# Performance work log

Measured on AMD Instinct MI355X. Metric: run time of the kernel, lower is better.

## Reference

```python
import jax, jax.numpy as jnp
import numpy as np

HIDDEN = 2048
FFN = 1024
NUM_EXPERTS = 64
TOP_K = 8
TOTAL_EXPERTS = NUM_EXPERTS + TOP_K  # trash-can experts appended


def setup_inputs() -> dict:
    key = jax.random.key(0)
    ks = jax.random.split(key, 5)
    hidden_states = jax.random.normal(ks[0], (4, 2048, HIDDEN), dtype=jnp.float32)
    # gate: [total_experts, hidden]
    gate_w = jax.random.normal(ks[1], (TOTAL_EXPERTS, HIDDEN), dtype=jnp.float32) * 0.02
    # OlmoeMLP (SwiGLU): gate_proj, up_proj: [E, hidden, ffn]; down_proj: [E, ffn, hidden]
    w_gate = jax.random.normal(ks[2], (NUM_EXPERTS, HIDDEN, FFN), dtype=jnp.float32) * 0.02
    w_up = jax.random.normal(ks[3], (NUM_EXPERTS, HIDDEN, FFN), dtype=jnp.float32) * 0.02
    w_down = jax.random.normal(ks[4], (NUM_EXPERTS, FFN, HIDDEN), dtype=jnp.float32) * 0.02
    return {"hidden_states": hidden_states, "gate_w": gate_w,
            "w_gate": w_gate, "w_up": w_up, "w_down": w_down}


def _moe_forward(hidden_states, gate_w, w_gate, w_up, w_down):
    b, s, h = hidden_states.shape
    x = hidden_states.reshape(-1, h)  # [T, H]
    router_logits = x @ gate_w.T  # [T, total_experts]
    routing_weights = jax.nn.softmax(router_logits.astype(jnp.float32), axis=-1)
    topk_w, topk_idx = jax.lax.top_k(routing_weights, TOP_K)  # [T, K]
    # norm_topk_prob = False -> no renorm
    topk_w = topk_w.astype(hidden_states.dtype)

    # Dense-equivalent combine honoring sparsity via per-expert mask-weighted sum:
    # combine_w[t, e] = sum of topk weights where topk_idx==e, zero for trash experts.
    onehot = jax.nn.one_hot(topk_idx, TOTAL_EXPERTS, dtype=topk_w.dtype)  # [T,K,E_tot]
    combine_w = jnp.einsum('tk,tke->te', topk_w, onehot)[:, :NUM_EXPERTS]  # [T,E]

    # Grouped expert compute (vectorized over experts).
    # For correctness baseline we compute each expert on all tokens and weight;
    # zero weights kill non-routed tokens (same math as gather/scatter).
    def one_expert(wg, wu, wd, w_col):
        inter = jax.nn.silu(x @ wg) * (x @ wu)  # [T, FFN]
        return (inter @ wd) * w_col[:, None]    # [T, H]

    out = jnp.zeros_like(x)
    # scan over experts to cap peak memory at one [T,FFN] intermediate
    def body(acc, args):
        wg, wu, wd, w_col = args
        return acc + one_expert(wg, wu, wd, w_col), None
    out, _ = jax.lax.scan(body, out, (w_gate, w_up, w_down, combine_w.T))
    return out.reshape(b, s, h), router_logits


def reference(hidden_states, gate_w, w_gate, w_up, w_down):
    return _moe_forward(hidden_states, gate_w, w_gate, w_up, w_down)
```

## Files before the change

### kernel.cpp

```cpp
#include <hip/hip_runtime.h>
#include <hip/hip_bf16.h>
#include <stdint.h>

#define T_TOK 8192
#define HID   2048
#define FFN   1024
#define NEXP  64
#define ETOT  72
#define NPAD  80
#define TOPK  8
#define NASSIGN (T_TOK*TOPK)

typedef unsigned short u16;
typedef __bf16 bf16;
typedef bf16 bf16x8 __attribute__((ext_vector_type(8)));
typedef float f32x4 __attribute__((ext_vector_type(4)));

typedef const __attribute__((address_space(1))) void* gp_t;
typedef __attribute__((address_space(3))) void* lp_t;

__device__ __forceinline__ void gload16(const void* g, void* lds) {
  __builtin_amdgcn_global_load_lds((gp_t)g, (lp_t)lds, 16, 0, 0);
}
__device__ __forceinline__ f32x4 mfma16(bf16x8 a, bf16x8 b, f32x4 c) {
  return __builtin_amdgcn_mfma_f32_16x16x32_bf16(a, b, c, 0, 0, 0);
}

union U8 { bf16 h[8]; uint4 u; };
union U2 { bf16 h[2]; unsigned int u; };

__global__ void k_prep_x(const float* __restrict__ x, u16* __restrict__ xh,
                         u16* __restrict__ xl, int n8) {
  int i = blockIdx.x * blockDim.x + threadIdx.x;
  int stride = gridDim.x * blockDim.x;
  for (; i < n8; i += stride) {
    const float4* p = (const float4*)(x + (size_t)i * 8);
    float4 a = p[0], b = p[1];
    float f[8] = {a.x,a.y,a.z,a.w,b.x,b.y,b.z,b.w};
    U8 hh, ll;
#pragma unroll
    for (int j = 0; j < 8; j++) {
      bf16 h = (bf16)f[j];
      hh.h[j] = h;
      ll.h[j] = (bf16)(f[j] - (float)h);
    }
    ((uint4*)xh)[i] = hh.u;
    ((uint4*)xl)[i] = ll.u;
  }
}

__global__ void k_prep_gate(const float* __restrict__ gw, u16* __restrict__ gh,
                            u16* __restrict__ gl) {
  int e = blockIdx.x;
  for (int k8 = threadIdx.x; k8 < HID/8; k8 += blockDim.x) {
    U8 hh, ll;
    if (e < ETOT) {
      const float4* p = (const float4*)(gw + (size_t)e*HID + k8*8);
      float4 a = p[0], b = p[1];
      float f[8] = {a.x,a.y,a.z,a.w,b.x,b.y,b.z,b.w};
#pragma unroll
      for (int j = 0; j < 8; j++) {
        bf16 h = (bf16)f[j]; hh.h[j] = h; ll.h[j] = (bf16)(f[j]-(float)h);
      }
    } else {
      hh.u = make_uint4(0,0,0,0); ll.u = make_uint4(0,0,0,0);
    }
    ((uint4*)gh)[(size_t)e*(HID/8) + k8] = hh.u;
    ((uint4*)gl)[(size_t)e*(HID/8) + k8] = ll.u;
  }
}

__global__ void k_convT(const float* __restrict__ src, u16* __restrict__ dst,
                        int R, int C) {
  int e = blockIdx.z;
  src += (size_t)e * R * C;
  dst += (size_t)e * R * C;
  int c0 = blockIdx.x * 64, r0 = blockIdx.y * 128;
  __shared__ u16 t[64 * 132];
  int tid = threadIdx.x;
  int rr = tid >> 4, cc = (tid & 15) * 4;
#pragma unroll
  for (int it = 0; it < 8; it++) {
    int r = it * 16 + rr;
    float4 v = *(const float4*)(src + (size_t)(r0 + r) * C + c0 + cc);
    const float* f = &v.x;
#pragma unroll
    for (int i = 0; i < 4; i++) {
      U2 u; u.h[0] = (bf16)f[i]; u.h[1] = (bf16)0.f;
      t[(cc + i) * 132 + r] = (u16)(u.u & 0xffffu);
    }
  }
  __syncthreads();
  int n = tid >> 2, kb = (tid & 3) * 32;
  u16* drow = dst + (size_t)(c0 + n) * R + r0 + kb;
  const u16* srow = &t[n * 132 + kb];
#pragma unroll
  for (int j = 0; j < 2; j++) {
    uint2 a = *(const uint2*)&srow[j*16 + 0];
    uint2 b = *(const uint2*)&srow[j*16 + 4];
    uint2 c = *(const uint2*)&srow[j*16 + 8];
    uint2 d = *(const uint2*)&srow[j*16 + 12];
    *(uint4*)&drow[j*16]     = make_uint4(a.x, a.y, b.x, b.y);
    *(uint4*)&drow[j*16 + 8] = make_uint4(c.x, c.y, d.x, d.y);
  }
}

__global__ void k_router(const u16* __restrict__ xh, const u16* __restrict__ xl,
                         const u16* __restrict__ gh, const u16* __restrict__ gl,
                         float* __restrict__ logits_out, int* __restrict__ tk_idx,
                         float* __restrict__ tk_w, int* __restrict__ counts) {
  __shared__ u16 la_h[64*32], la_l[64*32], lb_h[NPAD*32], lb_l[NPAD*32];
  __shared__ float llog[64*NPAD];
  int tid = threadIdx.x, lane = tid & 63, wid = tid >> 6;
  int t0 = blockIdx.x * 64;
  int rsub = lane >> 2, csub = lane & 3;
  f32x4 acc[5] = {};
#pragma unroll 1
  for (int k0 = 0; k0 < HID; k0 += 32) {
    int arow = wid*16 + rsub;
    gload16(xh + (size_t)(t0+arow)*HID + k0 + csub*8, &la_h[wid*512]);
    gload16(xl + (size_t)(t0+arow)*HID + k0 + csub*8, &la_l[wid*512]);
    int brow = wid*16 + rsub;
    gload16(gh + (size_t)brow*HID + k0 + csub*8, &lb_h[wid*512]);
    gload16(gl + (size_t)brow*HID + k0 + csub*8, &lb_l[wid*512]);
    if (wid == 0) gload16(gh + (size_t)(64+rsub)*HID + k0 + csub*8, &lb_h[4*512]);
    if (wid == 1) gload16(gl + (size_t)(64+rsub)*HID + k0 + csub*8, &lb_l[4*512]);
    __syncthreads();
    int ar = wid*16 + (lane & 15);
    int ks = lane >> 4;
    bf16x8 ah = *(const bf16x8*)&la_h[ar*32 + ks*8];
    bf16x8 al = *(const bf16x8*)&la_l[ar*32 + ks*8];
#pragma unroll
    for (int nf = 0; nf < 5; nf++) {
      int br = nf*16 + (lane & 15);
      bf16x8 bh = *(const bf16x8*)&lb_h[br*32 + ks*8];
      bf16x8 bl = *(const bf16x8*)&lb_l[br*32 + ks*8];
      acc[nf] = mfma16(ah, bh, acc[nf]);
      acc[nf] = mfma16(ah, bl, acc[nf]);
      acc[nf] = mfma16(al, bh, acc[nf]);
    }
    __syncthreads();
  }
  {
    int q = lane >> 4, c = lane & 15;
#pragma unroll
    for (int nf = 0; nf < 5; nf++)
#pragma unroll
      for (int r = 0; r < 4; r++)
        llog[(wid*16 + q*4 + r)*NPAD + nf*16 + c] = acc[nf][r];
  }
  __syncthreads();
  if (tid < 64) {
    int t = t0 + tid;
    float* lg = &llog[tid*NPAD];
    float m = -1e30f;
    for (int e = 0; e < ETOT; e++) {
      float v = lg[e];
      logits_out[(size_t)t*ETOT + e] = v;
      m = fmaxf(m, v);
    }
    float s = 0.f;
    for (int e = 0; e < ETOT; e++) s += __expf(lg[e] - m);
    uint64_t m0 = 0; unsigned int m1 = 0;
    for (int k = 0; k < TOPK; k++) {
      float best = -1e30f; int bi = 0;
      for (int e = 0; e < ETOT; e++) {
        bool used = (e < 64) ? ((m0 >> e) & 1) : ((m1 >> (e-64)) & 1);
        float v = lg[e];
        if (!used && v > best) { best = v; bi = e; }
      }
      if (bi < 64) m0 |= (1ull << bi); else m1 |= (1u << (bi-64));
      tk_idx[t*TOPK + k] = bi;
      tk_w[t*TOPK + k] = __expf(best - m) / s;
      if (bi < NEXP) atomicAdd(&counts[bi], 1);
    }
  }
}

__global__ void k_scan(const int* __restrict__ counts, int* __restrict__ offsets,
                       int* __restrict__ cursors) {
  if (threadIdx.x == 0) {
    int s = 0;
    for (int e = 0; e < NEXP; e++) { offsets[e] = s; cursors[e] = s; s += counts[e]; }
  }
}

__global__ void k_build(const int* __restrict__ tk_idx, const float* __restrict__ tk_w,
                        int* __restrict__ cursors, int* __restrict__ rows,
                        float* __restrict__ rwgt) {
  int t = blockIdx.x * blockDim.x + threadIdx.x;
  if (t >= T_TOK) return;
#pragma unroll
  for (int k = 0; k < TOPK; k++) {
    int e = tk_idx[t*TOPK + k];
    if (e < NEXP) {
      int p = atomicAdd(&cursors[e], 1);
      rows[p] = t;
      rwgt[p] = tk_w[t*TOPK + k];
    }
  }
}

__launch_bounds__(256, 3)
__global__ void k_expert_gu(const u16* __restrict__ xh, const u16* __restrict__ wgT,
                            const u16* __restrict__ wuT, const int* __restrict__ counts,
                            const int* __restrict__ offsets, const int* __restrict__ rows,
                            u16* __restrict__ inter) {
  int wgid = blockIdx.x;
  int xcd = wgid & 7, slot = wgid >> 3;
  int m = slot & 7, q = slot >> 3;
  int g = xcd * 64 + q;
  int e = g >> 3, nb = g & 7;
  int cnt = counts[e];
  if (cnt == 0) return;
  int off = offsets[e];
  int n0 = nb * 128;
  int tid = threadIdx.x, lane = tid & 63, wid = tid >> 6;
  int wm = (wid >> 1) * 64, wn = (wid & 1) * 64;
  __shared__ u16 la[128*32], lbg[128*32], lbu[128*32];
  __shared__ u16 lout[64*128];
  int rsub = lane >> 2, csub = lane & 3;
  int swzc = csub ^ ((rsub >> 1) & 3);
  int nr1 = wid*16 + rsub, nr2 = nr1 + 64;
  const u16* gb_g1 = wgT + ((size_t)e*FFN + n0 + nr1)*HID + swzc*8;
  const u16* gb_g2 = wgT + ((size_t)e*FFN + n0 + nr2)*HID + swzc*8;
  const u16* gb_u1 = wuT + ((size_t)e*FFN + n0 + nr1)*HID + swzc*8;
  const u16* gb_u2 = wuT + ((size_t)e*FFN + n0 + nr2)*HID + swzc*8;

  for (int m0 = m * 128; m0 < cnt; m0 += 1024) {
    int tok1 = (m0 + nr1 < cnt) ? rows[off + m0 + nr1] : 0;
    int tok2 = (m0 + nr2 < cnt) ? rows[off + m0 + nr2] : 0;
    const u16* ga1 = xh + (size_t)tok1*HID + swzc*8;
    const u16* ga2 = xh + (size_t)tok2*HID + swzc*8;
    f32x4 accg[4][4] = {}, accu[4][4] = {};
#pragma unroll 1
    for (int k0 = 0; k0 < HID; k0 += 32) {
      gload16(ga1 + k0, &la[wid*512]);
      gload16(ga2 + k0, &la[(wid+4)*512]);
      gload16(gb_g1 + k0, &lbg[wid*512]);
      gload16(gb_g2 + k0, &lbg[(wid+4)*512]);
      gload16(gb_u1 + k0, &lbu[wid*512]);
      gload16(gb_u2 + k0, &lbu[(wid+4)*512]);
      __syncthreads();
      bf16x8 afr[4], bgf[4], buf_[4];
#pragma unroll
      for (int i = 0; i < 4; i++) {
        int row = wm + i*16 + (lane & 15);
        int ch = (lane >> 4) ^ ((row >> 1) & 3);
        afr[i] = *(const bf16x8*)&la[row*32 + ch*8];
        int n = wn + i*16 + (lane & 15);
        int chb = (lane >> 4) ^ ((n >> 1) & 3);
        bgf[i]  = *(const bf16x8*)&lbg[n*32 + chb*8];
        buf_[i] = *(const bf16x8*)&lbu[n*32 + chb*8];
      }
#pragma unroll
      for (int nf = 0; nf < 4; nf++)
#pragma unroll
        for (int mf = 0; mf < 4; mf++) {
          accg[mf][nf] = mfma16(afr[mf], bgf[nf], accg[mf][nf]);
          accu[mf][nf] = mfma16(afr[mf], buf_[nf], accu[mf][nf]);
        }
      __syncthreads();
    }
#pragma unroll
    for (int pass = 0; pass < 2; pass++) {
      if ((wid >> 1) == pass) {
#pragma unroll
        for (int mf = 0; mf < 4; mf++)
#pragma unroll
          for (int nf = 0; nf < 4; nf++)
#pragma unroll
            for (int r = 0; r < 4; r++) {
              float gg = accg[mf][nf][r], uu = accu[mf][nf][r];
              float v = gg / (1.f + __expf(-gg)) * uu;
              int row = mf*16 + (lane >> 4)*4 + r;
              int col = wn + nf*16 + (lane & 15);
              U2 t; t.h[0] = (bf16)v; t.h[1] = (bf16)0.f;
              lout[row*128 + col] = (u16)(t.u & 0xffffu);
            }
      }
      __syncthreads();
      for (int idx = tid; idx < 1024; idx += 256) {
        int row = idx >> 4, c16 = idx & 15;
        int grow = m0 + pass*64 + row;
        if (grow < cnt) {
          uint4 v = *(const uint4*)&lout[row*128 + c16*8];
          *(uint4*)&inter[(size_t)(off + grow)*FFN + n0 + c16*8] = v;
        }
      }
      __syncthreads();
    }
  }
}

__launch_bounds__(256, 4)
__global__ void k_expert_down(const u16* __restrict__ inter, const u16* __restrict__ wdT,
                              const int* __restrict__ counts, const int* __restrict__ offsets,
                              const int* __restrict__ rows, const float* __restrict__ rwgt,
                              float* __restrict__ out) {
  int wgid = blockIdx.x;
  int xcd = wgid & 7, slot = wgid >> 3;
  int m = slot & 3, q = slot >> 2;
  int g = xcd * 128 + q;
  int e = g >> 4, nb = g & 15;
  int cnt = counts[e];
  if (cnt == 0) return;
  int off = offsets[e];
  int n0 = nb * 128;
  int tid = threadIdx.x, lane = tid & 63, wid = tid >> 6;
  int wm = (wid >> 1) * 64, wn = (wid & 1) * 64;
  __shared__ u16 la[128*32], lb[128*32];
  __shared__ int rows_l[128];
  __shared__ float rw_l[128];
  int rsub = lane >> 2, csub = lane & 3;
  int swzc = csub ^ ((rsub >> 1) & 3);
  int nr1 = wid*16 + rsub, nr2 = nr1 + 64;
  const u16* gb1 = wdT + ((size_t)e*HID + n0 + nr1)*FFN + swzc*8;
  const u16* gb2 = wdT + ((size_t)e*HID + n0 + nr2)*FFN + swzc*8;

  for (int m0 = m * 128; m0 < cnt; m0 += 512) {
    __syncthreads();
    if (tid < 128) {
      int r = m0 + tid;
      rows_l[tid] = (r < cnt) ? rows[off + r] : 0;
      rw_l[tid]   = (r < cnt) ? rwgt[off + r] : 0.f;
    }
    const u16* ga1 = inter + (size_t)(off + m0 + nr1)*FFN + swzc*8;
    const u16* ga2 = inter + (size_t)(off + m0 + nr2)*FFN + swzc*8;
    f32x4 acc[4][4] = {};
#pragma unroll 1
    for (int k0 = 0; k0 < FFN; k0 += 32) {
      gload16(ga1 + k0, &la[wid*512]);
      gload16(ga2 + k0, &la[(wid+4)*512]);
      gload16(gb1 + k0, &lb[wid*512]);
      gload16(gb2 + k0, &lb[(wid+4)*512]);
      __syncthreads();
      bf16x8 afr[4], bfr[4];
#pragma unroll
      for (int i = 0; i < 4; i++) {
        int row = wm + i*16 + (lane & 15);
        int ch = (lane >> 4) ^ ((row >> 1) & 3);
        afr[i] = *(const bf16x8*)&la[row*32 + ch*8];
        int n = wn + i*16 + (lane & 15);
        int chb = (lane >> 4) ^ ((n >> 1) & 3);
        bfr[i] = *(const bf16x8*)&lb[n*32 + chb*8];
      }
#pragma unroll
      for (int nf = 0; nf < 4; nf++)
#pragma unroll
        for (int mf = 0; mf < 4; mf++)
          acc[mf][nf] = mfma16(afr[mf], bfr[nf], acc[mf][nf]);
      __syncthreads();
    }
#pragma unroll
    for (int mf = 0; mf < 4; mf++)
#pragma unroll
      for (int nf = 0; nf < 4; nf++)
#pragma unroll
        for (int r = 0; r < 4; r++) {
          int row = wm + mf*16 + (lane >> 4)*4 + r;
          if (m0 + row < cnt) {
            int tok = rows_l[row];
            float w = rw_l[row];
            int col = n0 + wn + nf*16 + (lane & 15);
            atomicAdd(&out[(size_t)tok*HID + col], w * acc[mf][nf][r]);
          }
        }
  }
}

extern "C" void kernel_launch(void* const* d_in, const int* in_sizes, int n_in,
                              void* d_out, int out_size, void* d_ws, size_t ws_size,
                              hipStream_t stream) {
  const float* x      = (const float*)d_in[0];
  const float* gate_w = (const float*)d_in[1];
  const float* wg     = (const float*)d_in[2];
  const float* wu     = (const float*)d_in[3];
  const float* wd     = (const float*)d_in[4];
  float* out = (float*)d_out;
  float* logits_out = out + (size_t)T_TOK * HID;

  char* w = (char*)d_ws;
  u16* xh = (u16*)w;            w += (size_t)T_TOK*HID*2;
  u16* xl = (u16*)w;            w += (size_t)T_TOK*HID*2;
  u16* gh = (u16*)w;            w += (size_t)NPAD*HID*2;
  u16* gl = (u16*)w;            w += (size_t)NPAD*HID*2;
  int* tk_idx = (int*)w;        w += (size_t)T_TOK*TOPK*4;
  float* tk_w = (float*)w;      w += (size_t)T_TOK*TOPK*4;
  int* counts = (int*)w;        w += 256;
  int* offsets = (int*)w;       w += 256;
  int* cursors = (int*)w;       w += 256;
  int* rows = (int*)w;          w += (size_t)NASSIGN*4;
  float* rwgt = (float*)w;      w += (size_t)NASSIGN*4;
  u16* inter = (u16*)w;         w += ((size_t)NASSIGN + 256)*FFN*2;
  u16* wgT = (u16*)w;           w += (size_t)NEXP*FFN*HID*2;
  u16* wuT = (u16*)w;           w += (size_t)NEXP*FFN*HID*2;
  u16* wdT = (u16*)w;

  hipMemsetAsync(d_out, 0, (size_t)T_TOK*HID*4, stream);
  hipMemsetAsync(counts, 0, 256, stream);

  k_prep_x<<<2048, 256, 0, stream>>>(x, xh, xl, T_TOK*HID/8);
  k_prep_gate<<<NPAD, 256, 0, stream>>>(gate_w, gh, gl);
  k_router<<<T_TOK/64, 256, 0, stream>>>(xh, xl, gh, gl, logits_out, tk_idx, tk_w, counts);
  k_scan<<<1, 64, 0, stream>>>(counts, offsets, cursors);
  k_build<<<T_TOK/256, 256, 0, stream>>>(tk_idx, tk_w, cursors, rows, rwgt);

  k_convT<<<dim3(FFN/64, HID/128, NEXP), 256, 0, stream>>>(wg, wgT, HID, FFN);
  k_convT<<<dim3(FFN/64, HID/128, NEXP), 256, 0, stream>>>(wu, wuT, HID, FFN);
  k_convT<<<dim3(HID/64, FFN/128, NEXP), 256, 0, stream>>>(wd, wdT, FFN, HID);

  k_expert_gu<<<4096, 256, 0, stream>>>(xh, wgT, wuT, counts, offsets, rows, inter);
  k_expert_down<<<4096, 256, 0, stream>>>(inter, wdT, counts, offsets, rows, rwgt, out);
}
```

Measured before the change: 2.051 ms.

## Split fused gate/up expert GEMM into separate gate and up kernels

The fused gate+up expert kernel is split into two kernels. The first computes the gate projection and stores it as bf16 in the intermediate buffer. The second computes the up projection, reads the stored gate values back, and applies SiLU*up in place. Halving the accumulators and LDS per kernel lowers register pressure and allows higher occupancy (launch bounds go from 3 to 4 blocks). The cost is reading the activations twice, an extra round trip of the gate output through global memory, and rounding the gate to bf16 before SiLU.

New measurement: 1.959 ms. -4.4%, faster.

```diff
diff --git a/kernel.cpp b/kernel.cpp
--- a/kernel.cpp
+++ b/kernel.cpp
@@ -201,11 +201,10 @@
   }
 }
 
-__launch_bounds__(256, 3)
-__global__ void k_expert_gu(const u16* __restrict__ xh, const u16* __restrict__ wgT,
-                            const u16* __restrict__ wuT, const int* __restrict__ counts,
-                            const int* __restrict__ offsets, const int* __restrict__ rows,
-                            u16* __restrict__ inter) {
+__launch_bounds__(256, 4)
+__global__ void k_gate(const u16* __restrict__ xh, const u16* __restrict__ wT,
+                       const int* __restrict__ counts, const int* __restrict__ offsets,
+                       const int* __restrict__ rows, u16* __restrict__ gout) {
   int wgid = blockIdx.x;
   int xcd = wgid & 7, slot = wgid >> 3;
   int m = slot & 7, q = slot >> 3;
@@ -217,32 +216,30 @@
   int n0 = nb * 128;
   int tid = threadIdx.x, lane = tid & 63, wid = tid >> 6;
   int wm = (wid >> 1) * 64, wn = (wid & 1) * 64;
-  __shared__ u16 la[128*32], lbg[128*32], lbu[128*32];
-  __shared__ u16 lout[64*128];
+  __shared__ __align__(16) char smem[16384];
+  u16* la = (u16*)smem;
+  u16* lb = (u16*)(smem + 8192);
+  u16* lout = (u16*)smem;
   int rsub = lane >> 2, csub = lane & 3;
   int swzc = csub ^ ((rsub >> 1) & 3);
   int nr1 = wid*16 + rsub, nr2 = nr1 + 64;
-  const u16* gb_g1 = wgT + ((size_t)e*FFN + n0 + nr1)*HID + swzc*8;
-  const u16* gb_g2 = wgT + ((size_t)e*FFN + n0 + nr2)*HID + swzc*8;
-  const u16* gb_u1 = wuT + ((size_t)e*FFN + n0 + nr1)*HID + swzc*8;
-  const u16* gb_u2 = wuT + ((size_t)e*FFN + n0 + nr2)*HID + swzc*8;
+  const u16* gb1 = wT + ((size_t)e*FFN + n0 + nr1)*HID + swzc*8;
+  const u16* gb2 = wT + ((size_t)e*FFN + n0 + nr2)*HID + swzc*8;
 
   for (int m0 = m * 128; m0 < cnt; m0 += 1024) {
     int tok1 = (m0 + nr1 < cnt) ? rows[off + m0 + nr1] : 0;
     int tok2 = (m0 + nr2 < cnt) ? rows[off + m0 + nr2] : 0;
     const u16* ga1 = xh + (size_t)tok1*HID + swzc*8;
     const u16* ga2 = xh + (size_t)tok2*HID + swzc*8;
-    f32x4 accg[4][4] = {}, accu[4][4] = {};
+    f32x4 acc[4][4] = {};
 #pragma unroll 1
     for (int k0 = 0; k0 < HID; k0 += 32) {
       gload16(ga1 + k0, &la[wid*512]);
       gload16(ga2 + k0, &la[(wid+4)*512]);
-      gload16(gb_g1 + k0, &lbg[wid*512]);
-      gload16(gb_g2 + k0, &lbg[(wid+4)*512]);
-      gload16(gb_u1 + k0, &lbu[wid*512]);
-      gload16(gb_u2 + k0, &lbu[(wid+4)*512]);
-      __syncthreads();
-      bf16x8 afr[4], bgf[4], buf_[4];
+      gload16(gb1 + k0, &lb[wid*512]);
+      gload16(gb2 + k0, &lb[(wid+4)*512]);
+      __syncthreads();
+      bf16x8 afr[4], bfr[4];
 #pragma unroll
       for (int i = 0; i < 4; i++) {
         int row = wm + i*16 + (lane & 15);
@@ -250,16 +247,13 @@
         afr[i] = *(const bf16x8*)&la[row*32 + ch*8];
         int n = wn + i*16 + (lane & 15);
         int chb = (lane >> 4) ^ ((n >> 1) & 3);
-        bgf[i]  = *(const bf16x8*)&lbg[n*32 + chb*8];
-        buf_[i] = *(const bf16x8*)&lbu[n*32 + chb*8];
+        bfr[i] = *(const bf16x8*)&lb[n*32 + chb*8];
       }
 #pragma unroll
       for (int nf = 0; nf < 4; nf++)
 #pragma unroll
-        for (int mf = 0; mf < 4; mf++) {
-          accg[mf][nf] = mfma16(afr[mf], bgf[nf], accg[mf][nf]);
-          accu[mf][nf] = mfma16(afr[mf], buf_[nf], accu[mf][nf]);
-        }
+        for (int mf = 0; mf < 4; mf++)
+          acc[mf][nf] = mfma16(afr[mf], bfr[nf], acc[mf][nf]);
       __syncthreads();
     }
 #pragma unroll
@@ -271,10 +265,105 @@
           for (int nf = 0; nf < 4; nf++)
 #pragma unroll
             for (int r = 0; r < 4; r++) {
-              float gg = accg[mf][nf][r], uu = accu[mf][nf][r];
-              float v = gg / (1.f + __expf(-gg)) * uu;
               int row = mf*16 + (lane >> 4)*4 + r;
               int col = wn + nf*16 + (lane & 15);
+              U2 t; t.h[0] = (bf16)acc[mf][nf][r]; t.h[1] = (bf16)0.f;
+              lout[row*128 + col] = (u16)(t.u & 0xffffu);
+            }
+      }
+      __syncthreads();
+      for (int idx = tid; idx < 1024; idx += 256) {
+        int row = idx >> 4, c16 = idx & 15;
+        int grow = m0 + pass*64 + row;
+        if (grow < cnt) {
+          uint4 v = *(const uint4*)&lout[row*128 + c16*8];
+          *(uint4*)&gout[(size_t)(off + grow)*FFN + n0 + c16*8] = v;
+        }
+      }
+      __syncthreads();
+    }
+  }
+}
+
+__launch_bounds__(256, 4)
+__global__ void k_up(const u16* __restrict__ xh, const u16* __restrict__ wT,
+                     const int* __restrict__ counts, const int* __restrict__ offsets,
+                     const int* __restrict__ rows, u16* __restrict__ inter) {
+  int wgid = blockIdx.x;
+  int xcd = wgid & 7, slot = wgid >> 3;
+  int m = slot & 7, q = slot >> 3;
+  int g = xcd * 64 + q;
+  int e = g >> 3, nb = g & 7;
+  int cnt = counts[e];
+  if (cnt == 0) return;
+  int off = offsets[e];
+  int n0 = nb * 128;
+  int tid = threadIdx.x, lane = tid & 63, wid = tid >> 6;
+  int wm = (wid >> 1) * 64, wn = (wid & 1) * 64;
+  __shared__ __align__(16) char smem[32768];
+  u16* la = (u16*)smem;
+  u16* lb = (u16*)(smem + 8192);
+  u16* lg = (u16*)smem;
+  u16* lout = (u16*)(smem + 16384);
+  int rsub = lane >> 2, csub = lane & 3;
+  int swzc = csub ^ ((rsub >> 1) & 3);
+  int nr1 = wid*16 + rsub, nr2 = nr1 + 64;
+  const u16* gb1 = wT + ((size_t)e*FFN + n0 + nr1)*HID + swzc*8;
+  const u16* gb2 = wT + ((size_t)e*FFN + n0 + nr2)*HID + swzc*8;
+
+  for (int m0 = m * 128; m0 < cnt; m0 += 1024) {
+    int tok1 = (m0 + nr1 < cnt) ? rows[off + m0 + nr1] : 0;
+    int tok2 = (m0 + nr2 < cnt) ? rows[off + m0 + nr2] : 0;
+    const u16* ga1 = xh + (size_t)tok1*HID + swzc*8;
+    const u16* ga2 = xh + (size_t)tok2*HID + swzc*8;
+    f32x4 acc[4][4] = {};
+#pragma unroll 1
+    for (int k0 = 0; k0 < HID; k0 += 32) {
+      gload16(ga1 + k0, &la[wid*512]);
+      gload16(ga2 + k0, &la[(wid+4)*512]);
+      gload16(gb1 + k0, &lb[wid*512]);
+      gload16(gb2 + k0, &lb[(wid+4)*512]);
+      __syncthreads();
+      bf16x8 afr[4], bfr[4];
+#pragma unroll
+      for (int i = 0; i < 4; i++) {
+        int row = wm + i*16 + (lane & 15);
+        int ch = (lane >> 4) ^ ((row >> 1) & 3);
+        afr[i] = *(const bf16x8*)&la[row*32 + ch*8];
+        int n = wn + i*16 + (lane & 15);
+        int chb = (lane >> 4) ^ ((n >> 1) & 3);
+        bfr[i] = *(const bf16x8*)&lb[n*32 + chb*8];
+      }
+#pragma unroll
+      for (int nf = 0; nf < 4; nf++)
+#pragma unroll
+        for (int mf = 0; mf < 4; mf++)
+          acc[mf][nf] = mfma16(afr[mf], bfr[nf], acc[mf][nf]);
+      __syncthreads();
+    }
+#pragma unroll
+    for (int pass = 0; pass < 2; pass++) {
+      for (int idx = tid; idx < 1024; idx += 256) {
+        int row = idx >> 4, c16 = idx & 15;
+        int grow = m0 + pass*64 + row;
+        uint4 v = make_uint4(0,0,0,0);
+        if (grow < cnt)
+          v = *(const uint4*)&inter[(size_t)(off + grow)*FFN + n0 + c16*8];
+        *(uint4*)&lg[row*128 + c16*8] = v;
+      }
+      __syncthreads();
+      if ((wid >> 1) == pass) {
+#pragma unroll
+        for (int mf = 0; mf < 4; mf++)
+#pragma unroll
+          for (int nf = 0; nf < 4; nf++)
+#pragma unroll
+            for (int r = 0; r < 4; r++) {
+              int row = mf*16 + (lane >> 4)*4 + r;
+              int col = wn + nf*16 + (lane & 15);
+              U2 gv; gv.u = (unsigned int)lg[row*128 + col];
+              float gg = (float)gv.h[0];
+              float v = gg / (1.f + __expf(-gg)) * acc[mf][nf][r];
               U2 t; t.h[0] = (bf16)v; t.h[1] = (bf16)0.f;
               lout[row*128 + col] = (u16)(t.u & 0xffffu);
             }
@@ -410,6 +499,7 @@
   k_convT<<<dim3(FFN/64, HID/128, NEXP), 256, 0, stream>>>(wu, wuT, HID, FFN);
   k_convT<<<dim3(HID/64, FFN/128, NEXP), 256, 0, stream>>>(wd, wdT, FFN, HID);
 
-  k_expert_gu<<<4096, 256, 0, stream>>>(xh, wgT, wuT, counts, offsets, rows, inter);
+  k_gate<<<4096, 256, 0, stream>>>(xh, wgT, counts, offsets, rows, inter);
+  k_up<<<4096, 256, 0, stream>>>(xh, wuT, counts, offsets, rows, inter);
   k_expert_down<<<4096, 256, 0, stream>>>(inter, wdT, counts, offsets, rows, rwgt, out);
 }
```
